# Kernel optimization log

Measured on AMD Instinct MI355X. Metric: run time of the kernel, lower is better.

Reference implementation:

```python
import jax, jax.numpy as jnp
import numpy as np

B, K, D, R, V = 16384, 50, 64, 8, 100000
NEG = -1e9

def setup_inputs() -> dict:
    key = jax.random.key(0)
    ks = jax.random.split(key, 16)
    s = 0.1
    return {
        "nodes": jax.random.randint(ks[0], (B,), 0, V, dtype=jnp.int64 if jax.config.jax_enable_x64 else jnp.int32).astype(jnp.int32),
        "neigh_idx": jax.random.randint(ks[1], (B, K), 0, V).astype(jnp.int32),
        "neigh_len": jax.random.randint(ks[2], (B,), 0, 51).astype(jnp.int32),
        "neigh_labels": jax.random.uniform(ks[3], (B, K, R), dtype=jnp.float32),
        "u2e": jax.random.normal(ks[4], (V, D), dtype=jnp.float32) * s,
        "w1_W": jax.random.normal(ks[5], (D + R, D), dtype=jnp.float32) * s,
        "w1_b": jnp.zeros((D,), jnp.float32),
        "w2_W": jax.random.normal(ks[6], (D, D), dtype=jnp.float32) * s,
        "w2_b": jnp.zeros((D,), jnp.float32),
        "a1_W": jax.random.normal(ks[7], (2 * D, D), dtype=jnp.float32) * s,
        "a1_b": jnp.zeros((D,), jnp.float32),
        "a2_W": jax.random.normal(ks[8], (D, D), dtype=jnp.float32) * s,
        "a2_b": jnp.zeros((D,), jnp.float32),
        "a3_W": jax.random.normal(ks[9], (D, 1), dtype=jnp.float32) * s,
        "a3_b": jnp.zeros((1,), jnp.float32),
    }

def reference(nodes, neigh_idx, neigh_len, neigh_labels, u2e,
              w1_W, w1_b, w2_W, w2_b, a1_W, a1_b, a2_W, a2_b, a3_W, a3_b):
    u_rep = u2e[nodes]                      # [B, D] self embedding
    e_u = u2e[neigh_idx]                    # [B, K, D] neighbor embeddings (gather)
    x = jnp.concatenate([e_u, neigh_labels], axis=-1)          # [B, K, D+R]
    h = jax.nn.relu(x @ w1_W + w1_b)                            # w_r1
    o = jax.nn.relu(h @ w2_W + w2_b)                            # w_r2 -> o_history
    # attention: cat(o_history, u_rep repeated over neighbors)
    att_in = jnp.concatenate([o, jnp.broadcast_to(u_rep[:, None, :], o.shape)], axis=-1)  # [B,K,2D]
    a = jax.nn.relu(att_in @ a1_W + a1_b)
    a = jax.nn.relu(a @ a2_W + a2_b)
    scores = (a @ a3_W + a3_b)[..., 0]                          # [B, K]
    mask = jnp.arange(K)[None, :] < neigh_len[:, None]          # ragged validity mask
    scores = jnp.where(mask, scores, NEG)
    att = jax.nn.softmax(scores, axis=-1)                       # softmax over neighbors (dim=0 per node)
    att = jnp.where(mask, att, 0.0)
    agg = jnp.einsum('bk,bkd->bd', att, o)                      # attention-weighted aggregate
    # nodes with zero neighbors fall back to their own embedding
    return jnp.where((neigh_len > 0)[:, None], agg, u_rep)
```

## Files before the change

kernel.cpp:

```cpp
#include <hip/hip_runtime.h>

typedef __bf16 bf16_t;
typedef __bf16 bf16x8 __attribute__((ext_vector_type(8)));
typedef float f32x4 __attribute__((ext_vector_type(4)));

#define KN 50
#define B_TOT 16384
#define NITER 16
#define NBLK (B_TOT / NITER)

#define W1_OFF 0
#define W1_STR 104
#define W2_OFF 6656
#define W2_STR 72
#define A1_OFF 11264
#define A1_STR 136
#define A2_OFF 19968
#define A2_STR 72
#define W_ELEMS 24576
#define BIAS_BYTE_OFF (W_ELEMS * 2)
#define PACK_TOT (W_ELEMS + 321)

__global__ __launch_bounds__(256) void pack_weights_k(
    const float* __restrict__ w1, const float* __restrict__ w2,
    const float* __restrict__ a1, const float* __restrict__ a2,
    const float* __restrict__ b1, const float* __restrict__ b2,
    const float* __restrict__ ab1, const float* __restrict__ ab2,
    const float* __restrict__ a3w, const float* __restrict__ a3b,
    void* __restrict__ ws)
{
  int idx = blockIdx.x * 256 + threadIdx.x;
  if (idx >= PACK_TOT) return;
  bf16_t* wp = (bf16_t*)ws;
  float* bp = (float*)((char*)ws + BIAS_BYTE_OFF);
  if (idx < W2_OFF) {
    int n = idx / W1_STR, k = idx % W1_STR;
    wp[idx] = (bf16_t)((k < 72) ? w1[k * 64 + n] : 0.f);
  } else if (idx < A1_OFF) {
    int e = idx - W2_OFF; int n = e / W2_STR, k = e % W2_STR;
    wp[idx] = (bf16_t)((k < 64) ? w2[k * 64 + n] : 0.f);
  } else if (idx < A2_OFF) {
    int e = idx - A1_OFF; int n = e / A1_STR, k = e % A1_STR;
    wp[idx] = (bf16_t)((k < 128) ? a1[k * 64 + n] : 0.f);
  } else if (idx < W_ELEMS) {
    int e = idx - A2_OFF; int n = e / A2_STR, k = e % A2_STR;
    wp[idx] = (bf16_t)((k < 64) ? a2[k * 64 + n] : 0.f);
  } else {
    int e = idx - W_ELEMS;
    float v;
    if (e < 64) v = b1[e];
    else if (e < 128) v = b2[e - 64];
    else if (e < 192) v = ab1[e - 128];
    else if (e < 256) v = ab2[e - 192];
    else if (e < 320) v = a3w[e - 256];
    else v = a3b[0];
    bp[e] = v;
  }
}

__device__ __forceinline__ bf16x8 cvt8(float4 a, float4 b) {
  bf16x8 r;
  r[0] = (bf16_t)a.x; r[1] = (bf16_t)a.y; r[2] = (bf16_t)a.z; r[3] = (bf16_t)a.w;
  r[4] = (bf16_t)b.x; r[5] = (bf16_t)b.y; r[6] = (bf16_t)b.z; r[7] = (bf16_t)b.w;
  return r;
}

__device__ __forceinline__ float4 ldf4(const float* p) {
  return *reinterpret_cast<const float4*>(p);
}

__global__ __launch_bounds__(256, 2) void social_agg_k(
    const int* __restrict__ nodes,
    const int* __restrict__ nidx,
    const int* __restrict__ nlen,
    const float* __restrict__ labels,
    const float* __restrict__ u2e,
    const void* __restrict__ wsv,
    float* __restrict__ out)
{
  __shared__ __align__(16) bf16_t WL[W_ELEMS];
  __shared__ __align__(16) bf16_t Hs[64][72];
  __shared__ __align__(16) bf16_t Os[64][72];
  __shared__ float sco[64];
  __shared__ float part[4][64];

  const bf16_t* wp = (const bf16_t*)wsv;
  const float*  bp = (const float*)((const char*)wsv + BIAS_BYTE_OFF);

  const int tid  = threadIdx.x;
  const int lane = tid & 63;
  const int w    = tid >> 6;
  const int m0   = w * 16;
  const int lrow = lane & 15;
  const int lg   = lane >> 4;

  {
    const bf16x8* src = (const bf16x8*)wp;
    bf16x8* dst = (bf16x8*)WL;
#pragma unroll
    for (int c = 0; c < W_ELEMS / 8 / 256; ++c)
      dst[c * 256 + tid] = src[c * 256 + tid];
  }

  float bb1[4], bb2[4], ba1[4], ba2[4], a3c[4];
#pragma unroll
  for (int t = 0; t < 4; ++t) {
    const int col = t * 16 + lrow;
    bb1[t] = bp[col];       bb2[t] = bp[64 + col];
    ba1[t] = bp[128 + col]; ba2[t] = bp[192 + col];
    a3c[t] = bp[256 + col];
  }
  const float a3bias = bp[320];

  const int row  = m0 + lrow;
  const int crow = (row < KN) ? row : (KN - 1);
  const int b0   = blockIdx.x * NITER;

  int giC = nidx[(size_t)b0 * KN + crow];
  int ndC = nodes[b0];
  int lnC = nlen[b0];
  const float* xr = u2e + (size_t)giC * 64;
  float4 px0 = ldf4(xr + lg * 8);
  float4 px1 = ldf4(xr + lg * 8 + 4);
  float4 px2 = ldf4(xr + 32 + lg * 8);
  float4 px3 = ldf4(xr + 32 + lg * 8 + 4);
  float4 pl0 = {0.f, 0.f, 0.f, 0.f}, pl1 = {0.f, 0.f, 0.f, 0.f};
  if (lg == 0) {
    const float* lb = labels + ((size_t)b0 * KN + crow) * 8;
    pl0 = ldf4(lb); pl1 = ldf4(lb + 4);
  }
  const float* ur = u2e + (size_t)ndC * 64;
  float4 pu0 = ldf4(ur + lg * 8);
  float4 pu1 = ldf4(ur + lg * 8 + 4);
  float4 pu2 = ldf4(ur + 32 + lg * 8);
  float4 pu3 = ldf4(ur + 32 + lg * 8 + 4);
  int giN = nidx[(size_t)(b0 + 1) * KN + crow];
  int ndN = nodes[b0 + 1];
  int lnN = nlen[b0 + 1];

  __syncthreads();

  const f32x4 zero4 = {0.f, 0.f, 0.f, 0.f};

  for (int it = 0; it < NITER; ++it) {
    const int b = b0 + it;

    bf16x8 xa0 = cvt8(px0, px1);
    bf16x8 xa1 = cvt8(px2, px3);
    bf16x8 xa2 = cvt8(pl0, pl1);
    bf16x8 ua0 = cvt8(pu0, pu1);
    bf16x8 ua1 = cvt8(pu2, pu3);
    const int lenCur = lnC;
    const int ndCur  = ndC;

    if (it + 1 < NITER) {
      const float* xr2 = u2e + (size_t)giN * 64;
      px0 = ldf4(xr2 + lg * 8);
      px1 = ldf4(xr2 + lg * 8 + 4);
      px2 = ldf4(xr2 + 32 + lg * 8);
      px3 = ldf4(xr2 + 32 + lg * 8 + 4);
      if (lg == 0) {
        const float* lb2 = labels + ((size_t)(b + 1) * KN + crow) * 8;
        pl0 = ldf4(lb2); pl1 = ldf4(lb2 + 4);
      }
      const float* ur2 = u2e + (size_t)ndN * 64;
      pu0 = ldf4(ur2 + lg * 8);
      pu1 = ldf4(ur2 + lg * 8 + 4);
      pu2 = ldf4(ur2 + 32 + lg * 8);
      pu3 = ldf4(ur2 + 32 + lg * 8 + 4);
      lnC = lnN; ndC = ndN;
      const int b2 = (it + 2 < NITER) ? (b + 2) : b;
      giN = nidx[(size_t)b2 * KN + crow];
      ndN = nodes[b2];
      lnN = nlen[b2];
    }

    f32x4 acc[4];

#pragma unroll
    for (int t = 0; t < 4; ++t) acc[t] = zero4;
#pragma unroll
    for (int s = 0; s < 3; ++s) {
      bf16x8 af = (s == 0) ? xa0 : (s == 1) ? xa1 : xa2;
#pragma unroll
      for (int t = 0; t < 4; ++t) {
        bf16x8 bf_ = *reinterpret_cast<const bf16x8*>(
            &WL[W1_OFF + (t * 16 + lrow) * W1_STR + s * 32 + lg * 8]);
        acc[t] = __builtin_amdgcn_mfma_f32_16x16x32_bf16(af, bf_, acc[t], 0, 0, 0);
      }
    }
#pragma unroll
    for (int t = 0; t < 4; ++t) {
      const int col = t * 16 + lrow;
#pragma unroll
      for (int r = 0; r < 4; ++r) {
        float v = acc[t][r] + bb1[t];
        v = v > 0.f ? v : 0.f;
        Hs[m0 + lg * 4 + r][col] = (bf16_t)v;
      }
    }

#pragma unroll
    for (int t = 0; t < 4; ++t) acc[t] = zero4;
#pragma unroll
    for (int s = 0; s < 2; ++s) {
      bf16x8 af = *reinterpret_cast<const bf16x8*>(&Hs[m0 + lrow][s * 32 + lg * 8]);
#pragma unroll
      for (int t = 0; t < 4; ++t) {
        bf16x8 bf_ = *reinterpret_cast<const bf16x8*>(
            &WL[W2_OFF + (t * 16 + lrow) * W2_STR + s * 32 + lg * 8]);
        acc[t] = __builtin_amdgcn_mfma_f32_16x16x32_bf16(af, bf_, acc[t], 0, 0, 0);
      }
    }
    f32x4 osv[4];
#pragma unroll
    for (int t = 0; t < 4; ++t) {
      const int col = t * 16 + lrow;
#pragma unroll
      for (int r = 0; r < 4; ++r) {
        float v = acc[t][r] + bb2[t];
        v = v > 0.f ? v : 0.f;
        osv[t][r] = v;
        Os[m0 + lg * 4 + r][col] = (bf16_t)v;
      }
    }

#pragma unroll
    for (int t = 0; t < 4; ++t) acc[t] = zero4;
#pragma unroll
    for (int s = 0; s < 4; ++s) {
      bf16x8 af;
      if (s < 2)       af = *reinterpret_cast<const bf16x8*>(&Os[m0 + lrow][s * 32 + lg * 8]);
      else if (s == 2) af = ua0;
      else             af = ua1;
#pragma unroll
      for (int t = 0; t < 4; ++t) {
        bf16x8 bf_ = *reinterpret_cast<const bf16x8*>(
            &WL[A1_OFF + (t * 16 + lrow) * A1_STR + s * 32 + lg * 8]);
        acc[t] = __builtin_amdgcn_mfma_f32_16x16x32_bf16(af, bf_, acc[t], 0, 0, 0);
      }
    }
#pragma unroll
    for (int t = 0; t < 4; ++t) {
      const int col = t * 16 + lrow;
#pragma unroll
      for (int r = 0; r < 4; ++r) {
        float v = acc[t][r] + ba1[t];
        v = v > 0.f ? v : 0.f;
        Hs[m0 + lg * 4 + r][col] = (bf16_t)v;
      }
    }

#pragma unroll
    for (int t = 0; t < 4; ++t) acc[t] = zero4;
#pragma unroll
    for (int s = 0; s < 2; ++s) {
      bf16x8 af = *reinterpret_cast<const bf16x8*>(&Hs[m0 + lrow][s * 32 + lg * 8]);
#pragma unroll
      for (int t = 0; t < 4; ++t) {
        bf16x8 bf_ = *reinterpret_cast<const bf16x8*>(
            &WL[A2_OFF + (t * 16 + lrow) * A2_STR + s * 32 + lg * 8]);
        acc[t] = __builtin_amdgcn_mfma_f32_16x16x32_bf16(af, bf_, acc[t], 0, 0, 0);
      }
    }
    {
      float pr[4] = {0.f, 0.f, 0.f, 0.f};
#pragma unroll
      for (int t = 0; t < 4; ++t) {
#pragma unroll
        for (int r = 0; r < 4; ++r) {
          float v = acc[t][r] + ba2[t];
          v = v > 0.f ? v : 0.f;
          pr[r] += v * a3c[t];
        }
      }
#pragma unroll
      for (int r = 0; r < 4; ++r) {
#pragma unroll
        for (int m = 1; m < 16; m <<= 1) pr[r] += __shfl_xor(pr[r], m, 64);
      }
      if (lrow == 0) {
#pragma unroll
        for (int r = 0; r < 4; ++r) sco[m0 + lg * 4 + r] = pr[r] + a3bias;
      }
    }
    __syncthreads();

    float att4[4];
    {
      const bool valid = lane < lenCur;
      float s = valid ? sco[lane] : -1e30f;
      float m = s;
#pragma unroll
      for (int k = 1; k < 64; k <<= 1) m = fmaxf(m, __shfl_xor(m, k, 64));
      float e = valid ? __expf(s - m) : 0.f;
      float sm = e;
#pragma unroll
      for (int k = 1; k < 64; k <<= 1) sm += __shfl_xor(sm, k, 64);
      float att_own = (sm > 0.f) ? e / sm : 0.f;
#pragma unroll
      for (int r = 0; r < 4; ++r) att4[r] = __shfl(att_own, m0 + lg * 4 + r, 64);
    }

#pragma unroll
    for (int t = 0; t < 4; ++t) {
      float p = att4[0] * osv[t][0] + att4[1] * osv[t][1]
              + att4[2] * osv[t][2] + att4[3] * osv[t][3];
      p += __shfl_xor(p, 16, 64);
      p += __shfl_xor(p, 32, 64);
      if (lg == 0) part[w][t * 16 + lrow] = p;
    }
    __syncthreads();
    if (tid < 64) {
      float v = part[0][tid] + part[1][tid] + part[2][tid] + part[3][tid];
      if (lenCur > 0) out[(size_t)b * 64 + tid] = v;
      else            out[(size_t)b * 64 + tid] = u2e[(size_t)ndCur * 64 + tid];
    }
  }
}

extern "C" void kernel_launch(void* const* d_in, const int* in_sizes, int n_in,
                              void* d_out, int out_size, void* d_ws, size_t ws_size,
                              hipStream_t stream) {
  (void)in_sizes; (void)n_in; (void)out_size; (void)ws_size;
  const int*   nodes  = (const int*)d_in[0];
  const int*   nidx   = (const int*)d_in[1];
  const int*   nlen   = (const int*)d_in[2];
  const float* labels = (const float*)d_in[3];
  const float* u2e    = (const float*)d_in[4];
  const float* w1W    = (const float*)d_in[5];
  const float* w1b    = (const float*)d_in[6];
  const float* w2W    = (const float*)d_in[7];
  const float* w2b    = (const float*)d_in[8];
  const float* a1W    = (const float*)d_in[9];
  const float* a1b    = (const float*)d_in[10];
  const float* a2W    = (const float*)d_in[11];
  const float* a2b    = (const float*)d_in[12];
  const float* a3W    = (const float*)d_in[13];
  const float* a3b    = (const float*)d_in[14];
  float* out = (float*)d_out;

  pack_weights_k<<<(PACK_TOT + 255) / 256, 256, 0, stream>>>(
      w1W, w2W, a1W, a2W, w1b, w2b, a1b, a2b, a3W, a3b, d_ws);
  social_agg_k<<<NBLK, 256, 0, stream>>>(nodes, nidx, nlen, labels, u2e, d_ws, out);
}
```

Before: 228.8 us.

## Keep weights in registers, precompute self-embedding attention term, retile warps 2x2

Weight fragments now live in registers instead of being staged in LDS each block. A new prep kernel precomputes u_rep·a1W[64:] + a1_b per node, and the result seeds the attention accumulator, which removes half of the a1 K-dimension from the main kernel. Work is retiled so each wave handles 32 neighbors × 32 features with transposed MFMA operands. Block iterations per block double. This adds a separate launch, extra syncthreads between layers, and higher register pressure.

```diff
diff --git a/kernel.cpp b/kernel.cpp
--- a/kernel.cpp
+++ b/kernel.cpp
@@ -2,11 +2,12 @@
 
 typedef __bf16 bf16_t;
 typedef __bf16 bf16x8 __attribute__((ext_vector_type(8)));
+typedef __bf16 bf16x4v __attribute__((ext_vector_type(4)));
 typedef float f32x4 __attribute__((ext_vector_type(4)));
 
 #define KN 50
 #define B_TOT 16384
-#define NITER 16
+#define NITER 32
 #define NBLK (B_TOT / NITER)
 
 #define W1_OFF 0
@@ -20,6 +21,7 @@
 #define W_ELEMS 24576
 #define BIAS_BYTE_OFF (W_ELEMS * 2)
 #define PACK_TOT (W_ELEMS + 321)
+#define CU_BYTE_OFF 65536
 
 __global__ __launch_bounds__(256) void pack_weights_k(
     const float* __restrict__ w1, const float* __restrict__ w2,
@@ -58,6 +60,23 @@
   }
 }
 
+__global__ __launch_bounds__(256) void cu_prep_k(
+    const int* __restrict__ nodes, const float* __restrict__ u2e,
+    const float* __restrict__ a1W, const float* __restrict__ a1b,
+    void* __restrict__ ws)
+{
+  const int t = blockIdx.x * 256 + threadIdx.x;
+  const int bi = t >> 6;
+  const int f  = t & 63;
+  bf16_t* cu = (bf16_t*)((char*)ws + CU_BYTE_OFF);
+  const int nd = nodes[bi];
+  const float* ur = u2e + (size_t)nd * 64;
+  float s = a1b[f];
+#pragma unroll
+  for (int j = 0; j < 64; ++j) s += ur[j] * a1W[(64 + j) * 64 + f];
+  cu[(size_t)bi * 64 + f] = (bf16_t)s;
+}
+
 __device__ __forceinline__ bf16x8 cvt8(float4 a, float4 b) {
   bf16x8 r;
   r[0] = (bf16_t)a.x; r[1] = (bf16_t)a.y; r[2] = (bf16_t)a.z; r[3] = (bf16_t)a.w;
@@ -78,218 +97,245 @@
     const void* __restrict__ wsv,
     float* __restrict__ out)
 {
-  __shared__ __align__(16) bf16_t WL[W_ELEMS];
   __shared__ __align__(16) bf16_t Hs[64][72];
   __shared__ __align__(16) bf16_t Os[64][72];
-  __shared__ float sco[64];
-  __shared__ float part[4][64];
+  __shared__ float scp[2][64];
+  __shared__ float part[2][64];
 
   const bf16_t* wp = (const bf16_t*)wsv;
   const float*  bp = (const float*)((const char*)wsv + BIAS_BYTE_OFF);
+  const bf16_t* cu = (const bf16_t*)((const char*)wsv + CU_BYTE_OFF);
 
   const int tid  = threadIdx.x;
   const int lane = tid & 63;
   const int w    = tid >> 6;
-  const int m0   = w * 16;
+  const int mh   = w >> 1;
+  const int nh   = w & 1;
   const int lrow = lane & 15;
   const int lg   = lane >> 4;
 
-  {
-    const bf16x8* src = (const bf16x8*)wp;
-    bf16x8* dst = (bf16x8*)WL;
-#pragma unroll
-    for (int c = 0; c < W_ELEMS / 8 / 256; ++c)
-      dst[c * 256 + tid] = src[c * 256 + tid];
-  }
-
-  float bb1[4], bb2[4], ba1[4], ba2[4], a3c[4];
-#pragma unroll
-  for (int t = 0; t < 4; ++t) {
-    const int col = t * 16 + lrow;
-    bb1[t] = bp[col];       bb2[t] = bp[64 + col];
-    ba1[t] = bp[128 + col]; ba2[t] = bp[192 + col];
-    a3c[t] = bp[256 + col];
-  }
-  const float a3bias = bp[320];
-
-  const int row  = m0 + lrow;
-  const int crow = (row < KN) ? row : (KN - 1);
-  const int b0   = blockIdx.x * NITER;
-
-  int giC = nidx[(size_t)b0 * KN + crow];
+  bf16x8 w1f[2][3], w2f[2][2], a1f[2][2], a2f[2][2];
+#pragma unroll
+  for (int ft = 0; ft < 2; ++ft) {
+    const int n0 = (nh * 32 + ft * 16 + lrow);
+#pragma unroll
+    for (int s = 0; s < 3; ++s)
+      w1f[ft][s] = *reinterpret_cast<const bf16x8*>(wp + W1_OFF + n0 * W1_STR + s * 32 + lg * 8);
+#pragma unroll
+    for (int s = 0; s < 2; ++s) {
+      w2f[ft][s] = *reinterpret_cast<const bf16x8*>(wp + W2_OFF + n0 * W2_STR + s * 32 + lg * 8);
+      a1f[ft][s] = *reinterpret_cast<const bf16x8*>(wp + A1_OFF + n0 * A1_STR + s * 32 + lg * 8);
+      a2f[ft][s] = *reinterpret_cast<const bf16x8*>(wp + A2_OFF + n0 * A2_STR + s * 32 + lg * 8);
+    }
+  }
+
+  f32x4 bb1[2], bb2[2], ba2[2], a3c4[2];
+#pragma unroll
+  for (int ft = 0; ft < 2; ++ft) {
+    const int fb = nh * 32 + ft * 16 + lg * 4;
+    bb1[ft]  = *reinterpret_cast<const f32x4*>(bp + fb);
+    bb2[ft]  = *reinterpret_cast<const f32x4*>(bp + 64 + fb);
+    ba2[ft]  = *reinterpret_cast<const f32x4*>(bp + 192 + fb);
+    a3c4[ft] = *reinterpret_cast<const f32x4*>(bp + 256 + fb);
+  }
+
+  const int b0 = blockIdx.x * NITER;
+  int crow[2];
+#pragma unroll
+  for (int nt = 0; nt < 2; ++nt) {
+    const int nb = mh * 32 + nt * 16 + lrow;
+    crow[nt] = (nb < KN) ? nb : (KN - 1);
+  }
+
+  int giC[2], giN[2];
+  float4 px[2][4];
+  float4 plb[2][2] = {{{0,0,0,0},{0,0,0,0}},{{0,0,0,0},{0,0,0,0}}};
+  bf16x4v pcu[2];
   int ndC = nodes[b0];
   int lnC = nlen[b0];
-  const float* xr = u2e + (size_t)giC * 64;
-  float4 px0 = ldf4(xr + lg * 8);
-  float4 px1 = ldf4(xr + lg * 8 + 4);
-  float4 px2 = ldf4(xr + 32 + lg * 8);
-  float4 px3 = ldf4(xr + 32 + lg * 8 + 4);
-  float4 pl0 = {0.f, 0.f, 0.f, 0.f}, pl1 = {0.f, 0.f, 0.f, 0.f};
-  if (lg == 0) {
-    const float* lb = labels + ((size_t)b0 * KN + crow) * 8;
-    pl0 = ldf4(lb); pl1 = ldf4(lb + 4);
-  }
-  const float* ur = u2e + (size_t)ndC * 64;
-  float4 pu0 = ldf4(ur + lg * 8);
-  float4 pu1 = ldf4(ur + lg * 8 + 4);
-  float4 pu2 = ldf4(ur + 32 + lg * 8);
-  float4 pu3 = ldf4(ur + 32 + lg * 8 + 4);
-  int giN = nidx[(size_t)(b0 + 1) * KN + crow];
+#pragma unroll
+  for (int nt = 0; nt < 2; ++nt) {
+    giC[nt] = nidx[(size_t)b0 * KN + crow[nt]];
+    const float* xr = u2e + (size_t)giC[nt] * 64;
+    px[nt][0] = ldf4(xr + lg * 8);
+    px[nt][1] = ldf4(xr + lg * 8 + 4);
+    px[nt][2] = ldf4(xr + 32 + lg * 8);
+    px[nt][3] = ldf4(xr + 32 + lg * 8 + 4);
+    if (lg == 0) {
+      const float* lb = labels + ((size_t)b0 * KN + crow[nt]) * 8;
+      plb[nt][0] = ldf4(lb); plb[nt][1] = ldf4(lb + 4);
+    }
+  }
+#pragma unroll
+  for (int ft = 0; ft < 2; ++ft)
+    pcu[ft] = *reinterpret_cast<const bf16x4v*>(cu + (size_t)b0 * 64 + nh * 32 + ft * 16 + lg * 4);
   int ndN = nodes[b0 + 1];
   int lnN = nlen[b0 + 1];
-
-  __syncthreads();
-
-  const f32x4 zero4 = {0.f, 0.f, 0.f, 0.f};
+#pragma unroll
+  for (int nt = 0; nt < 2; ++nt)
+    giN[nt] = nidx[(size_t)(b0 + 1) * KN + crow[nt]];
 
   for (int it = 0; it < NITER; ++it) {
     const int b = b0 + it;
 
-    bf16x8 xa0 = cvt8(px0, px1);
-    bf16x8 xa1 = cvt8(px2, px3);
-    bf16x8 xa2 = cvt8(pl0, pl1);
-    bf16x8 ua0 = cvt8(pu0, pu1);
-    bf16x8 ua1 = cvt8(pu2, pu3);
+    bf16x8 xa[2][3];
+    f32x4 cu4[2];
+#pragma unroll
+    for (int nt = 0; nt < 2; ++nt) {
+      xa[nt][0] = cvt8(px[nt][0], px[nt][1]);
+      xa[nt][1] = cvt8(px[nt][2], px[nt][3]);
+      xa[nt][2] = cvt8(plb[nt][0], plb[nt][1]);
+    }
+#pragma unroll
+    for (int ft = 0; ft < 2; ++ft) {
+#pragma unroll
+      for (int r = 0; r < 4; ++r) cu4[ft][r] = (float)pcu[ft][r];
+    }
     const int lenCur = lnC;
     const int ndCur  = ndC;
 
     if (it + 1 < NITER) {
-      const float* xr2 = u2e + (size_t)giN * 64;
-      px0 = ldf4(xr2 + lg * 8);
-      px1 = ldf4(xr2 + lg * 8 + 4);
-      px2 = ldf4(xr2 + 32 + lg * 8);
-      px3 = ldf4(xr2 + 32 + lg * 8 + 4);
-      if (lg == 0) {
-        const float* lb2 = labels + ((size_t)(b + 1) * KN + crow) * 8;
-        pl0 = ldf4(lb2); pl1 = ldf4(lb2 + 4);
-      }
-      const float* ur2 = u2e + (size_t)ndN * 64;
-      pu0 = ldf4(ur2 + lg * 8);
-      pu1 = ldf4(ur2 + lg * 8 + 4);
-      pu2 = ldf4(ur2 + 32 + lg * 8);
-      pu3 = ldf4(ur2 + 32 + lg * 8 + 4);
+#pragma unroll
+      for (int nt = 0; nt < 2; ++nt) {
+        const float* xr2 = u2e + (size_t)giN[nt] * 64;
+        px[nt][0] = ldf4(xr2 + lg * 8);
+        px[nt][1] = ldf4(xr2 + lg * 8 + 4);
+        px[nt][2] = ldf4(xr2 + 32 + lg * 8);
+        px[nt][3] = ldf4(xr2 + 32 + lg * 8 + 4);
+        if (lg == 0) {
+          const float* lb2 = labels + ((size_t)(b + 1) * KN + crow[nt]) * 8;
+          plb[nt][0] = ldf4(lb2); plb[nt][1] = ldf4(lb2 + 4);
+        }
+      }
+#pragma unroll
+      for (int ft = 0; ft < 2; ++ft)
+        pcu[ft] = *reinterpret_cast<const bf16x4v*>(cu + (size_t)(b + 1) * 64 + nh * 32 + ft * 16 + lg * 4);
       lnC = lnN; ndC = ndN;
       const int b2 = (it + 2 < NITER) ? (b + 2) : b;
-      giN = nidx[(size_t)b2 * KN + crow];
+#pragma unroll
+      for (int nt = 0; nt < 2; ++nt)
+        giN[nt] = nidx[(size_t)b2 * KN + crow[nt]];
       ndN = nodes[b2];
       lnN = nlen[b2];
     }
 
-    f32x4 acc[4];
-
-#pragma unroll
-    for (int t = 0; t < 4; ++t) acc[t] = zero4;
-#pragma unroll
-    for (int s = 0; s < 3; ++s) {
-      bf16x8 af = (s == 0) ? xa0 : (s == 1) ? xa1 : xa2;
-#pragma unroll
-      for (int t = 0; t < 4; ++t) {
-        bf16x8 bf_ = *reinterpret_cast<const bf16x8*>(
-            &WL[W1_OFF + (t * 16 + lrow) * W1_STR + s * 32 + lg * 8]);
-        acc[t] = __builtin_amdgcn_mfma_f32_16x16x32_bf16(af, bf_, acc[t], 0, 0, 0);
-      }
-    }
-#pragma unroll
-    for (int t = 0; t < 4; ++t) {
-      const int col = t * 16 + lrow;
-#pragma unroll
-      for (int r = 0; r < 4; ++r) {
-        float v = acc[t][r] + bb1[t];
-        v = v > 0.f ? v : 0.f;
-        Hs[m0 + lg * 4 + r][col] = (bf16_t)v;
-      }
-    }
-
-#pragma unroll
-    for (int t = 0; t < 4; ++t) acc[t] = zero4;
-#pragma unroll
-    for (int s = 0; s < 2; ++s) {
-      bf16x8 af = *reinterpret_cast<const bf16x8*>(&Hs[m0 + lrow][s * 32 + lg * 8]);
-#pragma unroll
-      for (int t = 0; t < 4; ++t) {
-        bf16x8 bf_ = *reinterpret_cast<const bf16x8*>(
-            &WL[W2_OFF + (t * 16 + lrow) * W2_STR + s * 32 + lg * 8]);
-        acc[t] = __builtin_amdgcn_mfma_f32_16x16x32_bf16(af, bf_, acc[t], 0, 0, 0);
-      }
-    }
-    f32x4 osv[4];
-#pragma unroll
-    for (int t = 0; t < 4; ++t) {
-      const int col = t * 16 + lrow;
-#pragma unroll
-      for (int r = 0; r < 4; ++r) {
-        float v = acc[t][r] + bb2[t];
-        v = v > 0.f ? v : 0.f;
-        osv[t][r] = v;
-        Os[m0 + lg * 4 + r][col] = (bf16_t)v;
-      }
-    }
-
-#pragma unroll
-    for (int t = 0; t < 4; ++t) acc[t] = zero4;
-#pragma unroll
-    for (int s = 0; s < 4; ++s) {
-      bf16x8 af;
-      if (s < 2)       af = *reinterpret_cast<const bf16x8*>(&Os[m0 + lrow][s * 32 + lg * 8]);
-      else if (s == 2) af = ua0;
-      else             af = ua1;
-#pragma unroll
-      for (int t = 0; t < 4; ++t) {
-        bf16x8 bf_ = *reinterpret_cast<const bf16x8*>(
-            &WL[A1_OFF + (t * 16 + lrow) * A1_STR + s * 32 + lg * 8]);
-        acc[t] = __builtin_amdgcn_mfma_f32_16x16x32_bf16(af, bf_, acc[t], 0, 0, 0);
-      }
-    }
-#pragma unroll
-    for (int t = 0; t < 4; ++t) {
-      const int col = t * 16 + lrow;
-#pragma unroll
-      for (int r = 0; r < 4; ++r) {
-        float v = acc[t][r] + ba1[t];
-        v = v > 0.f ? v : 0.f;
-        Hs[m0 + lg * 4 + r][col] = (bf16_t)v;
-      }
-    }
-
-#pragma unroll
-    for (int t = 0; t < 4; ++t) acc[t] = zero4;
-#pragma unroll
-    for (int s = 0; s < 2; ++s) {
-      bf16x8 af = *reinterpret_cast<const bf16x8*>(&Hs[m0 + lrow][s * 32 + lg * 8]);
-#pragma unroll
-      for (int t = 0; t < 4; ++t) {
-        bf16x8 bf_ = *reinterpret_cast<const bf16x8*>(
-            &WL[A2_OFF + (t * 16 + lrow) * A2_STR + s * 32 + lg * 8]);
-        acc[t] = __builtin_amdgcn_mfma_f32_16x16x32_bf16(af, bf_, acc[t], 0, 0, 0);
-      }
-    }
+    f32x4 acc[2][2];
+
+#pragma unroll
+    for (int nt = 0; nt < 2; ++nt)
+#pragma unroll
+      for (int ft = 0; ft < 2; ++ft) acc[nt][ft] = bb1[ft];
+#pragma unroll
+    for (int s = 0; s < 3; ++s)
+#pragma unroll
+      for (int nt = 0; nt < 2; ++nt)
+#pragma unroll
+        for (int ft = 0; ft < 2; ++ft)
+          acc[nt][ft] = __builtin_amdgcn_mfma_f32_16x16x32_bf16(w1f[ft][s], xa[nt][s], acc[nt][ft], 0, 0, 0);
+#pragma unroll
+    for (int nt = 0; nt < 2; ++nt)
+#pragma unroll
+      for (int ft = 0; ft < 2; ++ft) {
+        bf16x4v h;
+#pragma unroll
+        for (int r = 0; r < 4; ++r) { float v = acc[nt][ft][r]; h[r] = (bf16_t)(v > 0.f ? v : 0.f); }
+        *reinterpret_cast<bf16x4v*>(&Hs[mh * 32 + nt * 16 + lrow][nh * 32 + ft * 16 + lg * 4]) = h;
+      }
+    __syncthreads();
+
+#pragma unroll
+    for (int nt = 0; nt < 2; ++nt)
+#pragma unroll
+      for (int ft = 0; ft < 2; ++ft) acc[nt][ft] = bb2[ft];
+#pragma unroll
+    for (int s = 0; s < 2; ++s)
+#pragma unroll
+      for (int nt = 0; nt < 2; ++nt) {
+        bf16x8 hb = *reinterpret_cast<const bf16x8*>(&Hs[mh * 32 + nt * 16 + lrow][s * 32 + lg * 8]);
+#pragma unroll
+        for (int ft = 0; ft < 2; ++ft)
+          acc[nt][ft] = __builtin_amdgcn_mfma_f32_16x16x32_bf16(w2f[ft][s], hb, acc[nt][ft], 0, 0, 0);
+      }
+    f32x4 osv[2][2];
+#pragma unroll
+    for (int nt = 0; nt < 2; ++nt)
+#pragma unroll
+      for (int ft = 0; ft < 2; ++ft) {
+        bf16x4v h;
+#pragma unroll
+        for (int r = 0; r < 4; ++r) {
+          float v = acc[nt][ft][r]; v = v > 0.f ? v : 0.f;
+          osv[nt][ft][r] = v; h[r] = (bf16_t)v;
+        }
+        *reinterpret_cast<bf16x4v*>(&Os[mh * 32 + nt * 16 + lrow][nh * 32 + ft * 16 + lg * 4]) = h;
+      }
+    __syncthreads();
+
+#pragma unroll
+    for (int nt = 0; nt < 2; ++nt)
+#pragma unroll
+      for (int ft = 0; ft < 2; ++ft) acc[nt][ft] = cu4[ft];
+#pragma unroll
+    for (int s = 0; s < 2; ++s)
+#pragma unroll
+      for (int nt = 0; nt < 2; ++nt) {
+        bf16x8 ob = *reinterpret_cast<const bf16x8*>(&Os[mh * 32 + nt * 16 + lrow][s * 32 + lg * 8]);
+#pragma unroll
+        for (int ft = 0; ft < 2; ++ft)
+          acc[nt][ft] = __builtin_amdgcn_mfma_f32_16x16x32_bf16(a1f[ft][s], ob, acc[nt][ft], 0, 0, 0);
+      }
+#pragma unroll
+    for (int nt = 0; nt < 2; ++nt)
+#pragma unroll
+      for (int ft = 0; ft < 2; ++ft) {
+        bf16x4v h;
+#pragma unroll
+        for (int r = 0; r < 4; ++r) { float v = acc[nt][ft][r]; h[r] = (bf16_t)(v > 0.f ? v : 0.f); }
+        *reinterpret_cast<bf16x4v*>(&Hs[mh * 32 + nt * 16 + lrow][nh * 32 + ft * 16 + lg * 4]) = h;
+      }
+    __syncthreads();
+
+#pragma unroll
+    for (int nt = 0; nt < 2; ++nt)
+#pragma unroll
+      for (int ft = 0; ft < 2; ++ft) acc[nt][ft] = ba2[ft];
+#pragma unroll
+    for (int s = 0; s < 2; ++s)
+#pragma unroll
+      for (int nt = 0; nt < 2; ++nt) {
+        bf16x8 hb = *reinterpret_cast<const bf16x8*>(&Hs[mh * 32 + nt * 16 + lrow][s * 32 + lg * 8]);
+#pragma unroll
+        for (int ft = 0; ft < 2; ++ft)
+          acc[nt][ft] = __builtin_amdgcn_mfma_f32_16x16x32_bf16(a2f[ft][s], hb, acc[nt][ft], 0, 0, 0);
+      }
     {
-      float pr[4] = {0.f, 0.f, 0.f, 0.f};
-#pragma unroll
-      for (int t = 0; t < 4; ++t) {
-#pragma unroll
-        for (int r = 0; r < 4; ++r) {
-          float v = acc[t][r] + ba2[t];
-          v = v > 0.f ? v : 0.f;
-          pr[r] += v * a3c[t];
-        }
-      }
-#pragma unroll
-      for (int r = 0; r < 4; ++r) {
-#pragma unroll
-        for (int m = 1; m < 16; m <<= 1) pr[r] += __shfl_xor(pr[r], m, 64);
-      }
-      if (lrow == 0) {
-#pragma unroll
-        for (int r = 0; r < 4; ++r) sco[m0 + lg * 4 + r] = pr[r] + a3bias;
+      float sc[2] = {0.f, 0.f};
+#pragma unroll
+      for (int nt = 0; nt < 2; ++nt)
+#pragma unroll
+        for (int ft = 0; ft < 2; ++ft)
+#pragma unroll
+          for (int r = 0; r < 4; ++r) {
+            float v = acc[nt][ft][r]; v = v > 0.f ? v : 0.f;
+            sc[nt] += v * a3c4[ft][r];
+          }
+#pragma unroll
+      for (int nt = 0; nt < 2; ++nt) {
+        sc[nt] += __shfl_xor(sc[nt], 16, 64);
+        sc[nt] += __shfl_xor(sc[nt], 32, 64);
+      }
+      if (lg == 0) {
+#pragma unroll
+        for (int nt = 0; nt < 2; ++nt)
+          scp[nh][mh * 32 + nt * 16 + lrow] = sc[nt];
       }
     }
     __syncthreads();
 
-    float att4[4];
+    float att4[2];
     {
       const bool valid = lane < lenCur;
-      float s = valid ? sco[lane] : -1e30f;
+      float s = valid ? (scp[0][lane] + scp[1][lane]) : -1e30f;
       float m = s;
 #pragma unroll
       for (int k = 1; k < 64; k <<= 1) m = fmaxf(m, __shfl_xor(m, k, 64));
@@ -299,22 +345,30 @@
       for (int k = 1; k < 64; k <<= 1) sm += __shfl_xor(sm, k, 64);
       float att_own = (sm > 0.f) ? e / sm : 0.f;
 #pragma unroll
-      for (int r = 0; r < 4; ++r) att4[r] = __shfl(att_own, m0 + lg * 4 + r, 64);
-    }
-
-#pragma unroll
-    for (int t = 0; t < 4; ++t) {
-      float p = att4[0] * osv[t][0] + att4[1] * osv[t][1]
-              + att4[2] * osv[t][2] + att4[3] * osv[t][3];
-      p += __shfl_xor(p, 16, 64);
-      p += __shfl_xor(p, 32, 64);
-      if (lg == 0) part[w][t * 16 + lrow] = p;
+      for (int nt = 0; nt < 2; ++nt)
+        att4[nt] = __shfl(att_own, mh * 32 + nt * 16 + lrow, 64);
+    }
+
+#pragma unroll
+    for (int ft = 0; ft < 2; ++ft) {
+      float pr[4];
+#pragma unroll
+      for (int r = 0; r < 4; ++r)
+        pr[r] = att4[0] * osv[0][ft][r] + att4[1] * osv[1][ft][r];
+#pragma unroll
+      for (int r = 0; r < 4; ++r) {
+#pragma unroll
+        for (int m = 1; m < 16; m <<= 1) pr[r] += __shfl_xor(pr[r], m, 64);
+      }
+      if (lrow == 0) {
+        float4 pv = {pr[0], pr[1], pr[2], pr[3]};
+        *reinterpret_cast<float4*>(&part[mh][nh * 32 + ft * 16 + lg * 4]) = pv;
+      }
     }
     __syncthreads();
     if (tid < 64) {
-      float v = part[0][tid] + part[1][tid] + part[2][tid] + part[3][tid];
-      if (lenCur > 0) out[(size_t)b * 64 + tid] = v;
-      else            out[(size_t)b * 64 + tid] = u2e[(size_t)ndCur * 64 + tid];
+      float v = part[0][tid] + part[1][tid];
+      out[(size_t)b * 64 + tid] = (lenCur > 0) ? v : u2e[(size_t)ndCur * 64 + tid];
     }
   }
 }
@@ -342,5 +396,6 @@
 
   pack_weights_k<<<(PACK_TOT + 255) / 256, 256, 0, stream>>>(
       w1W, w2W, a1W, a2W, w1b, w2b, a1b, a2b, a3W, a3b, d_ws);
+  cu_prep_k<<<(B_TOT * 64) / 256, 256, 0, stream>>>(nodes, u2e, a1W, a1b, d_ws);
   social_agg_k<<<NBLK, 256, 0, stream>>>(nodes, nidx, nlen, labels, u2e, d_ws, out);
 }
```

Result: slower. 245.0 us (+7.1%).
